# Kernel tuning notes

Hardware: AMD Instinct MI355X
Metric: run time of the kernel (lower is better)

## Reference

```python
import jax, jax.numpy as jnp
import numpy as np
from functools import partial

L, D, H, F, K, T = 8, 512, 8, 2048, 11, 2048
DK = D // H
PAD = (K - 1) // 2  # 5, matches pad_zeros width
SCALE = DK ** -0.5  # q,k each prescaled by d_k^-0.25 in the torch code


def setup_inputs() -> dict:
    key = jax.random.key(0)
    ks = jax.random.split(key, 16)
    s = 0.02
    return {
        "x": jax.random.normal(ks[0], (1, T, D), jnp.float32),
        "ln1_g": jnp.ones((L, D), jnp.float32),
        "ln1_b": jnp.zeros((L, D), jnp.float32),
        "Wqkv": jax.random.normal(ks[1], (L, D, 3 * D), jnp.float32) * s,
        "bqkv": jnp.zeros((L, 3 * D), jnp.float32),
        "fsmn_w": jax.random.normal(ks[2], (L, D, K), jnp.float32) * s,
        "Wout": jax.random.normal(ks[3], (L, D, D), jnp.float32) * s,
        "bout": jnp.zeros((L, D), jnp.float32),
        "ln2_g": jnp.ones((L, D), jnp.float32),
        "ln2_b": jnp.zeros((L, D), jnp.float32),
        "W1": jax.random.normal(ks[4], (L, D, F), jnp.float32) * s,
        "b1": jnp.zeros((L, F), jnp.float32),
        "W2": jax.random.normal(ks[5], (L, F, D), jnp.float32) * s,
        "b2": jnp.zeros((L, D), jnp.float32),
        "after_g": jnp.ones((D,), jnp.float32),
        "after_b": jnp.zeros((D,), jnp.float32),
    }


def layernorm(x, g, b, eps=1e-5):
    m = jnp.mean(x, axis=-1, keepdims=True)
    v = jnp.var(x, axis=-1, keepdims=True)
    return (x - m) * jax.lax.rsqrt(v + eps) * g + b


def fsmn(v, w):
    # v: [1, T, D]; depthwise conv1d, kernel K, zero-pad PAD each side (matches pad_zeros cat)
    vc = jnp.transpose(v, (0, 2, 1))  # [1, D, T]
    out = jax.lax.conv_general_dilated(
        vc, w[:, None, :], window_strides=(1,), padding=[(PAD, PAD)],
        feature_group_count=D, dimension_numbers=("NCH", "OIH", "NCH"))
    return jnp.transpose(out, (0, 2, 1)) + v  # fsmn_block(...) + v


def encoder_layer(x, p):
    (g1, b1_, Wqkv, bqkv, fw, Wout, bout, g2, b2_, W1, c1, W2, c2) = p
    x1 = layernorm(x, g1, b1_)
    qkv = jnp.einsum("btd,de->bte", x1, Wqkv) + bqkv  # [1, T, 3D]
    q, k, v = jnp.split(qkv, 3, axis=-1)
    qh = q.reshape(T, H, DK).transpose(1, 0, 2)  # [H, T, dk]
    kh = k.reshape(T, H, DK).transpose(1, 0, 2)
    vh = v.reshape(T, H, DK).transpose(1, 0, 2)
    scores = jnp.einsum("htd,hsd->hts", qh, kh) * SCALE  # [H, T, T]
    attn = jnp.einsum("hts,hsd->htd", jax.nn.softmax(scores, axis=-1), vh)
    attn = attn.transpose(1, 0, 2).reshape(1, T, D)
    attn = jnp.einsum("btd,de->bte", attn, Wout) + bout
    mem = fsmn(v, fw)
    x = x + attn + mem
    h = layernorm(x, g2, b2_)
    h = jax.nn.relu(jnp.einsum("btd,df->btf", h, W1) + c1)
    x = x + jnp.einsum("btf,fd->btd", h, W2) + c2
    return x, None


def reference(x, ln1_g, ln1_b, Wqkv, bqkv, fsmn_w, Wout, bout, ln2_g, ln2_b, W1, b1, W2, b2, after_g, after_b):
    params = (ln1_g, ln1_b, Wqkv, bqkv, fsmn_w, Wout, bout, ln2_g, ln2_b, W1, b1, W2, b2)
    x, _ = jax.lax.scan(encoder_layer, x, params)
    return layernorm(x, after_g, after_b)
```

## Files before the change

### kernel.cpp

```cpp
#include <hip/hip_runtime.h>

using u16 = unsigned short;
using u32 = unsigned int;

typedef __bf16 bf16x8 __attribute__((ext_vector_type(8)));
typedef float f32x4 __attribute__((ext_vector_type(4)));

typedef __attribute__((address_space(3))) u32 as3_u32;
typedef __attribute__((address_space(1))) const u32 as1_u32;

__device__ __forceinline__ u16 f2bf(float f) {
  u32 u = __builtin_bit_cast(u32, f);
  u = u + 0x7FFFu + ((u >> 16) & 1u);
  return (u16)(u >> 16);
}
__device__ __forceinline__ float bf2f(u16 h) {
  return __builtin_bit_cast(float, (u32)h << 16);
}

__device__ __forceinline__ void gload16(const u16* g, u16* l) {
  __builtin_amdgcn_global_load_lds((as1_u32*)g, (as3_u32*)l, 16, 0, 0);
}

__global__ __launch_bounds__(256) void transpose_f32_bf16(
    const float* __restrict__ in, u16* __restrict__ out, int R, int C) {
  __shared__ u16 tile[32][33];
  long zofs = (long)blockIdx.z * R * C;
  int c0 = blockIdx.x * 32, r0 = blockIdx.y * 32;
  for (int i = threadIdx.y; i < 32; i += 8)
    tile[i][threadIdx.x] = f2bf(in[zofs + (long)(r0 + i) * C + c0 + threadIdx.x]);
  __syncthreads();
  for (int i = threadIdx.y; i < 32; i += 8)
    out[zofs + (long)(c0 + i) * R + r0 + threadIdx.x] = tile[threadIdx.x][i];
}

template <int MI, int NI, int VT>
__global__ __launch_bounds__(256) void gemm_bt(
    const u16* __restrict__ A, int lda,
    const u16* __restrict__ B, int ldb,
    const float* __restrict__ bias,
    u16* __restrict__ outBf, int ldob,
    float* __restrict__ outF, int ldof, int accF,
    u16* __restrict__ vtOut,
    int M, int N, int K, int kChunks, float scale, int relu) {
  __shared__ u16 As[2][MI * 32 * 64];
  __shared__ u16 Bs[2][NI * 32 * 64];
  __shared__ u16 Ts[VT ? NI * 32 : 1][72];
  const int m0 = blockIdx.y * (MI * 32), n0 = blockIdx.x * (NI * 32);
  const int tid = threadIdx.x, lane = tid & 63, wid = tid >> 6;
  const int wr = (wid >> 1) * (MI * 16), wc = (wid & 1) * (NI * 16);
  const int r16 = lane & 15, kg = lane >> 4;

  const int lrow = lane >> 3;
  const int lchunk = (lane & 7) ^ lrow;

  f32x4 acc[MI][NI];
#pragma unroll
  for (int i = 0; i < MI; ++i)
#pragma unroll
    for (int j = 0; j < NI; ++j) acc[i][j] = f32x4{0.f, 0.f, 0.f, 0.f};

  const int kcs = K / kChunks;
  const int kbase = kcs * blockIdx.z;
  const int nkt = kcs / 64;

  auto STAGE = [&](int b, int k0) {
#pragma unroll
    for (int i = 0; i < MI; ++i) {
      const int r = i * 32 + wid * 8 + lrow;
      gload16(A + (long)(m0 + r) * lda + k0 + lchunk * 8,
              &As[b][wid * 512 + i * 2048]);
    }
#pragma unroll
    for (int j = 0; j < NI; ++j) {
      const int r = j * 32 + wid * 8 + lrow;
      gload16(B + (long)(n0 + r) * ldb + k0 + lchunk * 8,
              &Bs[b][wid * 512 + j * 2048]);
    }
  };

  STAGE(0, kbase);
  __syncthreads();

  for (int kt = 0; kt < nkt; ++kt) {
    const int cur = kt & 1;
    if (kt + 1 < nkt) STAGE(cur ^ 1, kbase + (kt + 1) * 64);

#pragma unroll
    for (int s = 0; s < 2; ++s) {
      bf16x8 af[MI], bfv[NI];
#pragma unroll
      for (int i = 0; i < MI; ++i) {
        const int r = wr + i * 16 + r16;
        af[i] = *reinterpret_cast<const bf16x8*>(
            &As[cur][r * 64 + (((s * 4 + kg) ^ (r & 7)) << 3)]);
      }
#pragma unroll
      for (int j = 0; j < NI; ++j) {
        const int r = wc + j * 16 + r16;
        bfv[j] = *reinterpret_cast<const bf16x8*>(
            &Bs[cur][r * 64 + (((s * 4 + kg) ^ (r & 7)) << 3)]);
      }
      __builtin_amdgcn_s_setprio(1);
#pragma unroll
      for (int i = 0; i < MI; ++i)
#pragma unroll
        for (int j = 0; j < NI; ++j)
          acc[i][j] = __builtin_amdgcn_mfma_f32_16x16x32_bf16(af[i], bfv[j], acc[i][j], 0, 0, 0);
      __builtin_amdgcn_s_setprio(0);
    }
    __syncthreads();
  }

  const int rg = (lane >> 4) * 4;
  const bool doVT = VT && (n0 >= 1024);
#pragma unroll
  for (int i = 0; i < MI; ++i) {
#pragma unroll
    for (int j = 0; j < NI; ++j) {
      int col = n0 + wc + j * 16 + r16;
      float bv = (bias && blockIdx.z == 0) ? bias[col] : 0.f;
#pragma unroll
      for (int r = 0; r < 4; ++r) {
        int row = m0 + wr + i * 16 + rg + r;
        float v = acc[i][j][r] * scale + bv;
        if (outF) {
          long idx = (long)row * ldof + col;
          if (accF) atomicAdd(&outF[idx], v);
          else outF[idx] = v;
        }
        if (outBf) {
          if (relu && v < 0.f) v = 0.f;
          u16 hv = f2bf(v);
          outBf[(long)row * ldob + col] = hv;
          if (doVT) Ts[wc + j * 16 + r16][wr + i * 16 + rg + r] = hv;
        }
      }
    }
  }

  if constexpr (VT) {
    if (doVT) {
      __syncthreads();
      const int d0 = n0 - 1024;
      constexpr int CH = MI * 4;
      constexpr int TOT = NI * 32 * CH;
#pragma unroll
      for (int c = 0; c < TOT / 256; ++c) {
        int idx = tid * (TOT / 256) + c;
        int drow = idx / CH, off = (idx % CH) * 8;
        *reinterpret_cast<uint4*>(vtOut + (long)(d0 + drow) * 2048 + m0 + off) =
            *reinterpret_cast<const uint4*>(&Ts[drow][off]);
      }
    }
  }
}

constexpr int AFP = 72;

__global__ __launch_bounds__(256, 4) void flash_attn_split(
    const u16* __restrict__ qkv, const u16* __restrict__ vT,
    u16* __restrict__ oPart, float* __restrict__ lPart) {
  __shared__ u16 Ks[2][64 * AFP];
  __shared__ u16 Vs[64 * AFP];
  __shared__ u16 Ps[4][16 * AFP];
  const int h = blockIdx.y;
  const int q0 = blockIdx.x * 64;
  const int split = blockIdx.z;
  const int tid = threadIdx.x;
  const int lane = tid & 63, wid = tid >> 6;
  const int r16 = lane & 15, kg8 = (lane >> 4) * 8;

  bf16x8 qa0, qa1;
  {
    union U { uint4 v; u16 hh[8]; } a, b;
    const u16* qrow = qkv + (long)(q0 + wid * 16 + r16) * 1536 + 64 * h;
    a.v = *reinterpret_cast<const uint4*>(qrow + kg8);
    b.v = *reinterpret_cast<const uint4*>(qrow + 32 + kg8);
#pragma unroll
    for (int i = 0; i < 8; ++i) {
      a.hh[i] = f2bf(bf2f(a.hh[i]) * 0.125f);
      b.hh[i] = f2bf(bf2f(b.hh[i]) * 0.125f);
    }
    qa0 = __builtin_bit_cast(bf16x8, a.v);
    qa1 = __builtin_bit_cast(bf16x8, b.v);
  }

  const int srow = tid >> 2;
  const int scol = (tid & 3) * 16;
  const u16* kgl = qkv + 512 + 64 * h + scol;
  const u16* vgl = vT + (long)(64 * h + srow) * 2048 + scol;

  uint4 kr0, kr1, vr0, vr1;
  auto LOAD = [&](int g) {
    const u16* kp = kgl + (long)(g * 64 + srow) * 1536;
    kr0 = *reinterpret_cast<const uint4*>(kp);
    kr1 = *reinterpret_cast<const uint4*>(kp + 8);
    const u16* vp = vgl + g * 64;
    vr0 = *reinterpret_cast<const uint4*>(vp);
    vr1 = *reinterpret_cast<const uint4*>(vp + 8);
  };
  auto STOREK = [&](int b) {
    *reinterpret_cast<uint4*>(&Ks[b][srow * AFP + scol]) = kr0;
    *reinterpret_cast<uint4*>(&Ks[b][srow * AFP + scol + 8]) = kr1;
  };
  auto STOREV = [&]() {
    *reinterpret_cast<uint4*>(&Vs[srow * AFP + scol]) = vr0;
    *reinterpret_cast<uint4*>(&Vs[srow * AFP + scol + 8]) = vr1;
  };

  f32x4 oacc[4];
#pragma unroll
  for (int j = 0; j < 4; ++j) oacc[j] = f32x4{0.f, 0.f, 0.f, 0.f};
  float lsum[4] = {0.f, 0.f, 0.f, 0.f};

  const int g0 = split * 8;
  LOAD(g0);
  STOREK(0);
  STOREV();
  __syncthreads();

  for (int t = 0; t < 8; ++t) {
    const int cur = t & 1;
    if (t < 7) LOAD(g0 + t + 1);

    f32x4 sacc[4];
#pragma unroll
    for (int j = 0; j < 4; ++j) sacc[j] = f32x4{0.f, 0.f, 0.f, 0.f};
    __builtin_amdgcn_s_setprio(1);
#pragma unroll
    for (int j = 0; j < 4; ++j) {
      bf16x8 b0 = *reinterpret_cast<const bf16x8*>(&Ks[cur][(j * 16 + r16) * AFP + kg8]);
      bf16x8 b1 = *reinterpret_cast<const bf16x8*>(&Ks[cur][(j * 16 + r16) * AFP + 32 + kg8]);
      sacc[j] = __builtin_amdgcn_mfma_f32_16x16x32_bf16(qa0, b0, sacc[j], 0, 0, 0);
      sacc[j] = __builtin_amdgcn_mfma_f32_16x16x32_bf16(qa1, b1, sacc[j], 0, 0, 0);
    }
    __builtin_amdgcn_s_setprio(0);

#pragma unroll
    for (int r = 0; r < 4; ++r) {
      float e0 = __expf(sacc[0][r]);
      float e1 = __expf(sacc[1][r]);
      float e2 = __expf(sacc[2][r]);
      float e3 = __expf(sacc[3][r]);
      lsum[r] += (e0 + e1) + (e2 + e3);
      int prow = (lane >> 4) * 4 + r;
      Ps[wid][prow * AFP + r16] = f2bf(e0);
      Ps[wid][prow * AFP + 16 + r16] = f2bf(e1);
      Ps[wid][prow * AFP + 32 + r16] = f2bf(e2);
      Ps[wid][prow * AFP + 48 + r16] = f2bf(e3);
    }

#pragma unroll
    for (int st = 0; st < 2; ++st) {
      bf16x8 pa = *reinterpret_cast<const bf16x8*>(&Ps[wid][r16 * AFP + st * 32 + kg8]);
      __builtin_amdgcn_s_setprio(1);
#pragma unroll
      for (int j = 0; j < 4; ++j) {
        bf16x8 bv = *reinterpret_cast<const bf16x8*>(&Vs[(j * 16 + r16) * AFP + st * 32 + kg8]);
        oacc[j] = __builtin_amdgcn_mfma_f32_16x16x32_bf16(pa, bv, oacc[j], 0, 0, 0);
      }
      __builtin_amdgcn_s_setprio(0);
    }

    if (t < 7) {
      STOREK(cur ^ 1);
      __syncthreads();
      STOREV();
      __syncthreads();
    }
  }

  const int rg = (lane >> 4) * 4;
#pragma unroll
  for (int r = 0; r < 4; ++r) {
    float ls = lsum[r];
#pragma unroll
    for (int o = 1; o < 16; o <<= 1) ls += __shfl_xor(ls, o);
    int row = q0 + wid * 16 + rg + r;
    if (r16 == 0) lPart[(long)(split * 8 + h) * 2048 + row] = ls;
#pragma unroll
    for (int j = 0; j < 4; ++j)
      oPart[(long)split * 2048 * 512 + (long)row * 512 + 64 * h + j * 16 + r16] =
          f2bf(oacc[j][r]);
  }
}

__global__ __launch_bounds__(256) void attn_norm_fsmn(
    const u16* __restrict__ oPart, const float* __restrict__ lPart,
    u16* __restrict__ attn, float* __restrict__ x,
    const u16* __restrict__ qkv, const float* __restrict__ fw) {
  const int t = blockIdx.x;
  const int d = threadIdx.x * 2;
  const int h = d >> 6;
  float l = 0.f;
#pragma unroll
  for (int s = 0; s < 4; ++s) l += lPart[(long)(s * 8 + h) * 2048 + t];
  float ox = 0.f, oy = 0.f;
#pragma unroll
  for (int s = 0; s < 4; ++s) {
    const u32 v = *reinterpret_cast<const u32*>(
        oPart + (long)s * 2048 * 512 + (long)t * 512 + d);
    ox += bf2f((u16)v);
    oy += bf2f((u16)(v >> 16));
  }
  const float inv = 1.f / l;
  u16* out = attn + (long)t * 512 + d;
  out[0] = f2bf(ox * inv);
  out[1] = f2bf(oy * inv);

  const u16* v = qkv + 1024 + d;
  float s0 = bf2f(v[(long)t * 1536]);
  float s1 = bf2f(v[(long)t * 1536 + 1]);
#pragma unroll
  for (int j = 0; j < 11; ++j) {
    int ts = t + j - 5;
    if (ts >= 0 && ts < 2048) {
      float w0 = fw[d * 11 + j], w1 = fw[(d + 1) * 11 + j];
      s0 += w0 * bf2f(v[(long)ts * 1536]);
      s1 += w1 * bf2f(v[(long)ts * 1536 + 1]);
    }
  }
  x[(long)t * 512 + d] += s0;
  x[(long)t * 512 + d + 1] += s1;
}

__device__ __forceinline__ void block_reduce2(float& s, float& ss) {
#pragma unroll
  for (int o = 32; o; o >>= 1) {
    s += __shfl_xor(s, o);
    ss += __shfl_xor(ss, o);
  }
  __shared__ float sm[8];
  int wid = threadIdx.x >> 6;
  if ((threadIdx.x & 63) == 0) {
    sm[wid] = s;
    sm[wid + 4] = ss;
  }
  __syncthreads();
  s = sm[0] + sm[1] + sm[2] + sm[3];
  ss = sm[4] + sm[5] + sm[6] + sm[7];
}

template <int OUTBF>
__global__ __launch_bounds__(256) void layernorm_k(
    const float* __restrict__ xin, const float* __restrict__ g,
    const float* __restrict__ bta, void* __restrict__ out) {
  const int row = blockIdx.x, tid = threadIdx.x;
  const float2 v = *reinterpret_cast<const float2*>(xin + (long)row * 512 + tid * 2);
  float s = v.x + v.y, ss = v.x * v.x + v.y * v.y;
  block_reduce2(s, ss);
  const float mean = s * (1.f / 512.f);
  const float var = ss * (1.f / 512.f) - mean * mean;
  const float inv = rsqrtf(var + 1e-5f);
  const float2 gg = *reinterpret_cast<const float2*>(g + tid * 2);
  const float2 bb = *reinterpret_cast<const float2*>(bta + tid * 2);
  const float y0 = (v.x - mean) * inv * gg.x + bb.x;
  const float y1 = (v.y - mean) * inv * gg.y + bb.y;
  if (OUTBF) {
    u16* o = (u16*)out + (long)row * 512 + tid * 2;
    o[0] = f2bf(y0);
    o[1] = f2bf(y1);
  } else {
    *reinterpret_cast<float2*>((float*)out + (long)row * 512 + tid * 2) =
        make_float2(y0, y1);
  }
}


extern "C" void kernel_launch(void* const* d_in, const int* in_sizes, int n_in,
                              void* d_out, int out_size, void* d_ws, size_t ws_size,
                              hipStream_t stream) {
  const float* in_x = (const float*)d_in[0];
  const float* ln1_g = (const float*)d_in[1];
  const float* ln1_b = (const float*)d_in[2];
  const float* Wqkv = (const float*)d_in[3];
  const float* bqkv = (const float*)d_in[4];
  const float* fsmn_w = (const float*)d_in[5];
  const float* Wout = (const float*)d_in[6];
  const float* bout = (const float*)d_in[7];
  const float* ln2_g = (const float*)d_in[8];
  const float* ln2_b = (const float*)d_in[9];
  const float* W1 = (const float*)d_in[10];
  const float* b1 = (const float*)d_in[11];
  const float* W2 = (const float*)d_in[12];
  const float* b2 = (const float*)d_in[13];
  const float* after_g = (const float*)d_in[14];
  const float* after_b = (const float*)d_in[15];

  const int T = 2048, D = 512, F = 2048, L = 8;

  char* p = (char*)d_ws;
  auto alloc = [&](size_t bytes) {
    char* r = p;
    p += (bytes + 255) & ~size_t(255);
    return r;
  };
  u16* WqkvT = (u16*)alloc(8L * 1536 * 512 * 2);
  u16* WoutT = (u16*)alloc(8L * 512 * 512 * 2);
  u16* W1T = (u16*)alloc(8L * 2048 * 512 * 2);
  u16* W2T = (u16*)alloc(8L * 512 * 2048 * 2);
  float* x = (float*)alloc((long)T * D * 4);
  u16* x1 = (u16*)alloc((long)T * D * 2);
  u16* qkv = (u16*)alloc((long)T * 1536 * 2);
  u16* vT = (u16*)alloc((long)D * T * 2);
  u16* attn = (u16*)alloc((long)T * D * 2);
  u16* hb = (u16*)alloc((long)T * F * 2);
  u16* oPart = (u16*)alloc(4L * T * D * 2);
  float* lPart = (float*)alloc(4L * 8 * T * 4);

  hipMemcpyAsync(x, in_x, (long)T * D * 4, hipMemcpyDeviceToDevice, stream);
  dim3 tb(32, 8);
  transpose_f32_bf16<<<dim3(1536 / 32, 512 / 32, 8), tb, 0, stream>>>(Wqkv, WqkvT, 512, 1536);
  transpose_f32_bf16<<<dim3(512 / 32, 512 / 32, 8), tb, 0, stream>>>(Wout, WoutT, 512, 512);
  transpose_f32_bf16<<<dim3(2048 / 32, 512 / 32, 8), tb, 0, stream>>>(W1, W1T, 512, 2048);
  transpose_f32_bf16<<<dim3(512 / 32, 2048 / 32, 8), tb, 0, stream>>>(W2, W2T, 2048, 512);

  for (int l = 0; l < L; ++l) {
    layernorm_k<1><<<T, 256, 0, stream>>>(x, ln1_g + 512 * l, ln1_b + 512 * l, x1);
    gemm_bt<2, 2, 1><<<dim3(24, 32, 1), 256, 0, stream>>>(
        x1, 512, WqkvT + (long)l * 1536 * 512, 512, bqkv + 1536 * l,
        qkv, 1536, (float*)nullptr, 0, 0, vT, T, 1536, 512, 1, 1.f, 0);
    flash_attn_split<<<dim3(32, 8, 4), 256, 0, stream>>>(qkv, vT, oPart, lPart);
    attn_norm_fsmn<<<T, 256, 0, stream>>>(oPart, lPart, attn, x, qkv,
                                          fsmn_w + (long)l * 512 * 11);
    gemm_bt<2, 2, 0><<<dim3(8, 32, 4), 256, 0, stream>>>(
        attn, 512, WoutT + (long)l * 512 * 512, 512, bout + 512 * l,
        (u16*)nullptr, 0, x, 512, 1, (u16*)nullptr, T, 512, 512, 4, 1.f, 0);
    layernorm_k<1><<<T, 256, 0, stream>>>(x, ln2_g + 512 * l, ln2_b + 512 * l, x1);
    gemm_bt<2, 2, 0><<<dim3(32, 32, 1), 256, 0, stream>>>(
        x1, 512, W1T + (long)l * 2048 * 512, 512, b1 + 2048 * l,
        hb, 2048, (float*)nullptr, 0, 0, (u16*)nullptr, T, 2048, 512, 1, 1.f, 1);
    gemm_bt<2, 2, 0><<<dim3(8, 32, 4), 256, 0, stream>>>(
        hb, 2048, W2T + (long)l * 512 * 2048, 2048, b2 + 512 * l,
        (u16*)nullptr, 0, x, 512, 1, (u16*)nullptr, T, 512, 2048, 4, 1.f, 0);
  }
  layernorm_k<0><<<T, 256, 0, stream>>>(x, after_g, after_b, (float*)d_out);
}
```

Before: 852.4 us.

## Fuse split-attention combine into Wout GEMM and FSMN into attention launch

Removes the separate attn_norm_fsmn kernel. The split-K attention partial sums and softmax normalisation are now combined while loading the A operand of a dedicated Wout GEMM, which atomically adds into x. The FSMN depthwise conv runs as an extra z-slice of blocks inside the flash attention launch, with weights held in registers and 8 timesteps per block. This saves a kernel launch and the attn intermediate round trip, at the cost of heavier A-tile loads (4 partials per element) and FSMN blocks sharing the attention grid.

After: 877.9 us. 1.03x slower.

```diff
diff --git a/kernel.cpp b/kernel.cpp
--- a/kernel.cpp
+++ b/kernel.cpp
@@ -156,18 +156,165 @@
   }
 }
 
+__global__ __launch_bounds__(256) void gemm_wout(
+    const u16* __restrict__ oPart, const float* __restrict__ lPart,
+    const u16* __restrict__ B,
+    const float* __restrict__ bias, float* __restrict__ x) {
+  __shared__ u16 As[2][64 * 64];
+  __shared__ u16 Bs[2][64 * 64];
+  const int m0 = blockIdx.y * 64, n0 = blockIdx.x * 64;
+  const int tid = threadIdx.x, lane = tid & 63, wid = tid >> 6;
+  const int wr = (wid >> 1) * 32, wc = (wid & 1) * 32;
+  const int r16 = lane & 15, kg = lane >> 4;
+  const int lrow = lane >> 3;
+  const int lchunk = (lane & 7) ^ lrow;
+
+  const int arow = tid >> 2;
+  const int ac16 = (tid & 3) * 16;
+
+  uint4 a4[4][2];
+  float lv[4];
+  auto LOADA = [&](int k0) {
+    const int h = k0 >> 6;
+#pragma unroll
+    for (int s = 0; s < 4; ++s) {
+      const u16* op = oPart + ((long)s * 2048 + m0 + arow) * 512 + k0 + ac16;
+      a4[s][0] = *reinterpret_cast<const uint4*>(op);
+      a4[s][1] = *reinterpret_cast<const uint4*>(op + 8);
+      lv[s] = lPart[(long)(s * 8 + h) * 2048 + m0 + arow];
+    }
+  };
+  auto STOREA = [&](int b) {
+    const float inv = 1.f / ((lv[0] + lv[1]) + (lv[2] + lv[3]));
+#pragma unroll
+    for (int c = 0; c < 2; ++c) {
+      u16 out8[8];
+#pragma unroll
+      for (int e = 0; e < 8; ++e) {
+        float acc = 0.f;
+#pragma unroll
+        for (int s = 0; s < 4; ++s)
+          acc += bf2f(reinterpret_cast<const u16*>(&a4[s][c])[e]);
+        out8[e] = f2bf(acc * inv);
+      }
+      const int cc = (tid & 3) * 2 + c;
+      *reinterpret_cast<uint4*>(&As[b][arow * 64 + ((cc ^ (arow & 7)) << 3)]) =
+          *reinterpret_cast<const uint4*>(out8);
+    }
+  };
+  auto STAGEB = [&](int b, int k0) {
+#pragma unroll
+    for (int j = 0; j < 2; ++j) {
+      const int r = j * 32 + wid * 8 + lrow;
+      gload16(B + (long)(n0 + r) * 512 + k0 + lchunk * 8,
+              &Bs[b][wid * 512 + j * 2048]);
+    }
+  };
+
+  f32x4 acc[2][2];
+#pragma unroll
+  for (int i = 0; i < 2; ++i)
+#pragma unroll
+    for (int j = 0; j < 2; ++j) acc[i][j] = f32x4{0.f, 0.f, 0.f, 0.f};
+
+  const int kbase = 128 * blockIdx.z;
+  LOADA(kbase);
+  STAGEB(0, kbase);
+  STOREA(0);
+  __syncthreads();
+
+  for (int kt = 0; kt < 2; ++kt) {
+    const int cur = kt & 1;
+    if (kt == 0) {
+      LOADA(kbase + 64);
+      STAGEB(1, kbase + 64);
+    }
+
+#pragma unroll
+    for (int s = 0; s < 2; ++s) {
+      bf16x8 af[2], bfv[2];
+#pragma unroll
+      for (int i = 0; i < 2; ++i) {
+        const int r = wr + i * 16 + r16;
+        af[i] = *reinterpret_cast<const bf16x8*>(
+            &As[cur][r * 64 + (((s * 4 + kg) ^ (r & 7)) << 3)]);
+      }
+#pragma unroll
+      for (int j = 0; j < 2; ++j) {
+        const int r = wc + j * 16 + r16;
+        bfv[j] = *reinterpret_cast<const bf16x8*>(
+            &Bs[cur][r * 64 + (((s * 4 + kg) ^ (r & 7)) << 3)]);
+      }
+      __builtin_amdgcn_s_setprio(1);
+#pragma unroll
+      for (int i = 0; i < 2; ++i)
+#pragma unroll
+        for (int j = 0; j < 2; ++j)
+          acc[i][j] = __builtin_amdgcn_mfma_f32_16x16x32_bf16(af[i], bfv[j], acc[i][j], 0, 0, 0);
+      __builtin_amdgcn_s_setprio(0);
+    }
+    if (kt == 0) STOREA(1);
+    __syncthreads();
+  }
+
+  const int rg = (lane >> 4) * 4;
+#pragma unroll
+  for (int i = 0; i < 2; ++i) {
+#pragma unroll
+    for (int j = 0; j < 2; ++j) {
+      int col = n0 + wc + j * 16 + r16;
+      float bv = (blockIdx.z == 0) ? bias[col] : 0.f;
+#pragma unroll
+      for (int r = 0; r < 4; ++r) {
+        int row = m0 + wr + i * 16 + rg + r;
+        atomicAdd(&x[(long)row * 512 + col], acc[i][j][r] + bv);
+      }
+    }
+  }
+}
+
 constexpr int AFP = 72;
 
 __global__ __launch_bounds__(256, 4) void flash_attn_split(
     const u16* __restrict__ qkv, const u16* __restrict__ vT,
-    u16* __restrict__ oPart, float* __restrict__ lPart) {
+    u16* __restrict__ oPart, float* __restrict__ lPart,
+    float* __restrict__ x, const float* __restrict__ fw) {
   __shared__ u16 Ks[2][64 * AFP];
   __shared__ u16 Vs[64 * AFP];
   __shared__ u16 Ps[4][16 * AFP];
+  const int split = blockIdx.z;
+  const int tid = threadIdx.x;
+
+  if (split == 4) {
+    const int cell = blockIdx.y * 32 + blockIdx.x;
+    const int d = tid * 2;
+    const u16* v = qkv + 1024 + d;
+    float w0[11], w1[11];
+#pragma unroll
+    for (int j = 0; j < 11; ++j) {
+      w0[j] = fw[d * 11 + j];
+      w1[j] = fw[(d + 1) * 11 + j];
+    }
+    for (int rr = 0; rr < 8; ++rr) {
+      const int t = cell * 8 + rr;
+      float s0 = bf2f(v[(long)t * 1536]);
+      float s1 = bf2f(v[(long)t * 1536 + 1]);
+#pragma unroll
+      for (int j = 0; j < 11; ++j) {
+        int ts = t + j - 5;
+        if (ts >= 0 && ts < 2048) {
+          s0 += w0[j] * bf2f(v[(long)ts * 1536]);
+          s1 += w1[j] * bf2f(v[(long)ts * 1536 + 1]);
+        }
+      }
+      x[(long)t * 512 + d] += s0;
+      x[(long)t * 512 + d + 1] += s1;
+    }
+    return;
+  }
+
   const int h = blockIdx.y;
   const int q0 = blockIdx.x * 64;
-  const int split = blockIdx.z;
-  const int tid = threadIdx.x;
   const int lane = tid & 63, wid = tid >> 6;
   const int r16 = lane & 15, kg8 = (lane >> 4) * 8;
 
@@ -284,45 +431,6 @@
       oPart[(long)split * 2048 * 512 + (long)row * 512 + 64 * h + j * 16 + r16] =
           f2bf(oacc[j][r]);
   }
-}
-
-__global__ __launch_bounds__(256) void attn_norm_fsmn(
-    const u16* __restrict__ oPart, const float* __restrict__ lPart,
-    u16* __restrict__ attn, float* __restrict__ x,
-    const u16* __restrict__ qkv, const float* __restrict__ fw) {
-  const int t = blockIdx.x;
-  const int d = threadIdx.x * 2;
-  const int h = d >> 6;
-  float l = 0.f;
-#pragma unroll
-  for (int s = 0; s < 4; ++s) l += lPart[(long)(s * 8 + h) * 2048 + t];
-  float ox = 0.f, oy = 0.f;
-#pragma unroll
-  for (int s = 0; s < 4; ++s) {
-    const u32 v = *reinterpret_cast<const u32*>(
-        oPart + (long)s * 2048 * 512 + (long)t * 512 + d);
-    ox += bf2f((u16)v);
-    oy += bf2f((u16)(v >> 16));
-  }
-  const float inv = 1.f / l;
-  u16* out = attn + (long)t * 512 + d;
-  out[0] = f2bf(ox * inv);
-  out[1] = f2bf(oy * inv);
-
-  const u16* v = qkv + 1024 + d;
-  float s0 = bf2f(v[(long)t * 1536]);
-  float s1 = bf2f(v[(long)t * 1536 + 1]);
-#pragma unroll
-  for (int j = 0; j < 11; ++j) {
-    int ts = t + j - 5;
-    if (ts >= 0 && ts < 2048) {
-      float w0 = fw[d * 11 + j], w1 = fw[(d + 1) * 11 + j];
-      s0 += w0 * bf2f(v[(long)ts * 1536]);
-      s1 += w1 * bf2f(v[(long)ts * 1536 + 1]);
-    }
-  }
-  x[(long)t * 512 + d] += s0;
-  x[(long)t * 512 + d + 1] += s1;
 }
 
 __device__ __forceinline__ void block_reduce2(float& s, float& ss) {
@@ -404,7 +512,6 @@
   u16* x1 = (u16*)alloc((long)T * D * 2);
   u16* qkv = (u16*)alloc((long)T * 1536 * 2);
   u16* vT = (u16*)alloc((long)D * T * 2);
-  u16* attn = (u16*)alloc((long)T * D * 2);
   u16* hb = (u16*)alloc((long)T * F * 2);
   u16* oPart = (u16*)alloc(4L * T * D * 2);
   float* lPart = (float*)alloc(4L * 8 * T * 4);
@@ -421,12 +528,10 @@
     gemm_bt<2, 2, 1><<<dim3(24, 32, 1), 256, 0, stream>>>(
         x1, 512, WqkvT + (long)l * 1536 * 512, 512, bqkv + 1536 * l,
         qkv, 1536, (float*)nullptr, 0, 0, vT, T, 1536, 512, 1, 1.f, 0);
-    flash_attn_split<<<dim3(32, 8, 4), 256, 0, stream>>>(qkv, vT, oPart, lPart);
-    attn_norm_fsmn<<<T, 256, 0, stream>>>(oPart, lPart, attn, x, qkv,
-                                          fsmn_w + (long)l * 512 * 11);
-    gemm_bt<2, 2, 0><<<dim3(8, 32, 4), 256, 0, stream>>>(
-        attn, 512, WoutT + (long)l * 512 * 512, 512, bout + 512 * l,
-        (u16*)nullptr, 0, x, 512, 1, (u16*)nullptr, T, 512, 512, 4, 1.f, 0);
+    flash_attn_split<<<dim3(32, 8, 5), 256, 0, stream>>>(
+        qkv, vT, oPart, lPart, x, fsmn_w + (long)l * 512 * 11);
+    gemm_wout<<<dim3(8, 32, 4), 256, 0, stream>>>(
+        oPart, lPart, WoutT + (long)l * 512 * 512, bout + 512 * l, x);
     layernorm_k<1><<<T, 256, 0, stream>>>(x, ln2_g + 512 * l, ln2_b + 512 * l, x1);
     gemm_bt<2, 2, 0><<<dim3(32, 32, 1), 256, 0, stream>>>(
         x1, 512, W1T + (long)l * 2048 * 512, 512, b1 + 2048 * l,
```
